# Kernel optimization log

Measured on AMD Instinct MI355X. Metric: run time of the kernel, lower is better.

Reference implementation:

```python
import jax, jax.numpy as jnp
import numpy as np

B, S, D, H = 2, 2048, 1024, 16
HD = D // H

def setup_inputs() -> dict:
    key = jax.random.key(0)
    ks = jax.random.split(key, 6)
    X = jax.random.normal(ks[0], (B, S, D), dtype=jnp.float32)
    mask = jax.random.randint(ks[1], (B, 1, S, S), 0, 2, dtype=jnp.int32)
    scale = 1.0 / np.sqrt(D)
    Wq = jax.random.normal(ks[2], (D, D), dtype=jnp.float32) * scale
    Wk = jax.random.normal(ks[3], (D, D), dtype=jnp.float32) * scale
    Wv = jax.random.normal(ks[4], (D, D), dtype=jnp.float32) * scale
    Wo = jax.random.normal(ks[5], (D, D), dtype=jnp.float32) * scale
    return {"X": X, "mask": mask, "Wq": Wq, "Wk": Wk, "Wv": Wv, "Wo": Wo}

def reference(X, mask, Wq, Wk, Wv, Wo):
    b, s, d = X.shape
    # torch nn.Linear(bias=False): y = x @ W.T, W is [out, in]
    def split_heads(Y):
        return Y.reshape(b, s, H, HD).transpose(0, 2, 1, 3)  # [b,h,s,hd]
    Q = split_heads(X @ Wq.T)
    K = split_heads(X @ Wk.T)
    V = split_heads(X @ Wv.T)
    scores = jnp.einsum('bhqd,bhkd->bhqk', Q, K) / jnp.sqrt(jnp.float32(HD))
    # Faithful to original: masked positions filled with -1e-09 (sic)
    scores = jnp.where(mask == 0, jnp.float32(-1e-09), scores)
    # dropout p=0.0 -> identity (applied to scores pre-softmax in original)
    weights = jax.nn.softmax(scores, axis=-1)
    out = jnp.einsum('bhqk,bhkd->bhqd', weights, V)  # [b,h,s,hd]
    out = out.transpose(0, 2, 1, 3).reshape(b, s, d)
    return out @ Wo.T
```

## Files before the change

### kernel.cpp

```cpp
#include <hip/hip_runtime.h>
#include <hip/hip_bf16.h>

using short8  = __attribute__((ext_vector_type(8))) short;
using f32x4   = __attribute__((ext_vector_type(4))) float;

#if __has_builtin(__builtin_amdgcn_exp2f)
#define EXP2(x) __builtin_amdgcn_exp2f(x)
#else
#define EXP2(x) __expf(0.6931471805599453f*(x))
#endif

__device__ __forceinline__ unsigned short f2bf(float x){
  union { float f; unsigned u; } c; c.f = x;
  unsigned u = c.u + 0x7FFFu + ((c.u >> 16) & 1u);
  return (unsigned short)(u >> 16);
}

__device__ __forceinline__ unsigned pack_bf16_rn(float a, float b){
  __hip_bfloat162 t = __float22bfloat162_rn(make_float2(a, b));
  unsigned u; __builtin_memcpy(&u, &t, 4);
  return u;
}

__global__ __launch_bounds__(256) void prep(const float* __restrict__ X, const int* __restrict__ Mk,
                                            const float* __restrict__ Wq, const float* __restrict__ Wk,
                                            const float* __restrict__ Wv, const float* __restrict__ Wo,
                                            unsigned short* __restrict__ Xb, unsigned short* __restrict__ Wqkv,
                                            unsigned short* __restrict__ Wob, unsigned long long* __restrict__ Mbits)
{
  const int bid = blockIdx.x, tid = threadIdx.x;
  if (bid < 8192){
    const float* src; unsigned short* dst; float scale; int i;
    if (bid < 4096)      { src = X;  dst = Xb;             scale = 1.0f;          i = bid*1024 + tid*4; }
    else if (bid < 5120) { src = Wq; dst = Wqkv;           scale = 0.18033688f;   i = (bid-4096)*1024 + tid*4; }
    else if (bid < 6144) { src = Wk; dst = Wqkv + 1048576; scale = 1.0f;          i = (bid-5120)*1024 + tid*4; }
    else if (bid < 7168) { src = Wv; dst = Wqkv + 2097152; scale = 1.0f;          i = (bid-6144)*1024 + tid*4; }
    else                 { src = Wo; dst = Wob;            scale = 1.0f;          i = (bid-7168)*1024 + tid*4; }
    float4 v = *(const float4*)(src + i);
    ushort4 o;
    o.x = f2bf(v.x * scale); o.y = f2bf(v.y * scale);
    o.z = f2bf(v.z * scale); o.w = f2bf(v.w * scale);
    *(ushort4*)(dst + i) = o;
  } else {
    int row = bid - 8192;
    const int* src = Mk + (size_t)row * 2048;
    unsigned long long* dst = Mbits + (size_t)row * 32;
    int w = tid >> 6, l = tid & 63;
    #pragma unroll
    for (int p = 0; p < 8; p++){
      int v = src[w*512 + p*64 + l];
      unsigned long long bm = __ballot(v != 0);
      if (l == 0) dst[w*8 + p] = bm;
    }
  }
}

__device__ __forceinline__ void stage16(const unsigned short* g, unsigned short* l){
  __builtin_amdgcn_global_load_lds(
      (const __attribute__((address_space(1))) void*)g,
      (__attribute__((address_space(3))) void*)l, 16, 0, 0);
}

__global__ __launch_bounds__(256) void gemm_qkv(const unsigned short* __restrict__ A,
                                                const unsigned short* __restrict__ B,
                                                unsigned short* __restrict__ C,
                                                unsigned short* __restrict__ Vg)
{
  __shared__ unsigned short As[128*32];
  __shared__ unsigned short Bs[128*32];
  const int tid = threadIdx.x;
  const int wave = tid >> 6, lane = tid & 63, l16 = lane & 15, quad = lane >> 4;
  const int id = blockIdx.x, xcd = id & 7, m = id >> 3;
  const int bm = (m / 3) * 128, bn = (xcd * 3 + (m % 3)) * 128;
  const int wm = (wave >> 1) * 64, wn = (wave & 1) * 64;
  const int K = 1024;

  f32x4 acc[4][4] = {};
  for (int k0 = 0; k0 < K; k0 += 32){
    #pragma unroll
    for (int c = 0; c < 2; c++){
      int idx = c * 256 + tid;
      int row = idx >> 2, g = (idx & 3) * 8;
      stage16(A + (size_t)(bm + row) * K + k0 + g, &As[idx * 8]);
      stage16(B + (size_t)(bn + row) * K + k0 + g, &Bs[idx * 8]);
    }
    __syncthreads();
    short8 af[4], bf[4];
    #pragma unroll
    for (int i = 0; i < 4; i++) af[i] = *(const short8*)&As[(wm + i*16 + l16)*32 + quad*8];
    #pragma unroll
    for (int j = 0; j < 4; j++) bf[j] = *(const short8*)&Bs[(wn + j*16 + l16)*32 + quad*8];
    #pragma unroll
    for (int i = 0; i < 4; i++)
      #pragma unroll
      for (int j = 0; j < 4; j++)
        acc[i][j] = __builtin_amdgcn_mfma_f32_16x16x32_bf16(af[i], bf[j], acc[i][j], 0, 0, 0);
    __syncthreads();
  }

  if (bn < 2048){
    #pragma unroll
    for (int i = 0; i < 4; i++){
      int mrow = bm + wm + i*16 + quad*4;
      #pragma unroll
      for (int j = 0; j < 4; j++){
        int ncol = bn + wn + j*16 + l16;
        #pragma unroll
        for (int r = 0; r < 4; r++)
          C[(size_t)(mrow + r) * 3072 + ncol] = f2bf(acc[i][j][r]);
      }
    }
  } else {
    #pragma unroll
    for (int i = 0; i < 4; i++){
      int srow = bm + wm + i*16 + quad*4;
      int b = srow >> 11, s = srow & 2047;
      #pragma unroll
      for (int j = 0; j < 4; j++){
        int c = bn - 2048 + wn + j*16 + l16;
        int h = c >> 6, d = c & 63;
        ushort4 o;
        o.x = f2bf(acc[i][j][0]); o.y = f2bf(acc[i][j][1]);
        o.z = f2bf(acc[i][j][2]); o.w = f2bf(acc[i][j][3]);
        *(ushort4*)&Vg[((size_t)(b*16 + h)*64 + d) * 2048 + s] = o;
      }
    }
  }
}

__global__ __launch_bounds__(256) void gemm_out(const unsigned short* __restrict__ A,
                                                const unsigned short* __restrict__ B,
                                                float* __restrict__ Cf)
{
  __shared__ unsigned short As[128*32];
  __shared__ unsigned short Bs[64*32];
  const int tid = threadIdx.x;
  const int wave = tid >> 6, lane = tid & 63, l16 = lane & 15, quad = lane >> 4;
  const int id = blockIdx.x, xcd = id & 7, m = id >> 3;
  const int bm = (m >> 1) * 128, bn = (xcd * 2 + (m & 1)) * 64;
  const int wm = (wave >> 1) * 64, wn = (wave & 1) * 32;
  const int K = 1024, N = 1024;

  f32x4 acc[4][2] = {};
  for (int k0 = 0; k0 < K; k0 += 32){
    #pragma unroll
    for (int c = 0; c < 2; c++){
      int idx = c * 256 + tid;
      int row = idx >> 2, g = (idx & 3) * 8;
      stage16(A + (size_t)(bm + row) * K + k0 + g, &As[idx * 8]);
    }
    stage16(B + (size_t)(bn + (tid >> 2)) * K + k0 + (tid & 3) * 8, &Bs[tid * 8]);
    __syncthreads();
    short8 af[4], bf[2];
    #pragma unroll
    for (int i = 0; i < 4; i++) af[i] = *(const short8*)&As[(wm + i*16 + l16)*32 + quad*8];
    #pragma unroll
    for (int j = 0; j < 2; j++) bf[j] = *(const short8*)&Bs[(wn + j*16 + l16)*32 + quad*8];
    #pragma unroll
    for (int i = 0; i < 4; i++)
      #pragma unroll
      for (int j = 0; j < 2; j++)
        acc[i][j] = __builtin_amdgcn_mfma_f32_16x16x32_bf16(af[i], bf[j], acc[i][j], 0, 0, 0);
    __syncthreads();
  }
  #pragma unroll
  for (int i = 0; i < 4; i++){
    int mrow = bm + wm + i*16 + quad*4;
    #pragma unroll
    for (int j = 0; j < 2; j++){
      int ncol = bn + wn + j*16 + l16;
      #pragma unroll
      for (int r = 0; r < 4; r++)
        Cf[(size_t)(mrow + r) * N + ncol] = acc[i][j][r];
    }
  }
}

__global__ __launch_bounds__(256, 4) void attn(const unsigned short* __restrict__ QKV,
                                               const unsigned short* __restrict__ Vg,
                                               const unsigned short* __restrict__ mask16,
                                               unsigned short* __restrict__ O)
{
  __shared__ char smem[40960];
  unsigned short* Ks = (unsigned short*)smem;
  unsigned short* Vt = (unsigned short*)(smem + 16384);
  unsigned short* Ps = (unsigned short*)(smem + 32768);
  float* lsums = (float*)smem;

  const int tid = threadIdx.x, wave = tid >> 6, lane = tid & 63;
  const int l16 = lane & 15, quad = lane >> 4;
  const int id = blockIdx.x;
  const int xcd = id & 7, m = id >> 3;
  const int bh = xcd * 4 + (m >> 5);
  const int qblk = (m & 31) * 64;
  const int b = bh >> 4, h = bh & 15;
  const unsigned short* Qg  = QKV + (size_t)b * 2048 * 3072 + h * 64;
  const unsigned short* Kg  = Qg + 1024;
  const unsigned short* Vgb = Vg + (size_t)bh * 64 * 2048;

  const unsigned short* mp[4];
  #pragma unroll
  for (int nt = 0; nt < 4; nt++)
    mp[nt] = mask16 + (size_t)(b*2048 + qblk + nt*16 + l16) * 128 + wave;

  short8 qf[4][2];
  #pragma unroll
  for (int nt = 0; nt < 4; nt++)
    #pragma unroll
    for (int ks = 0; ks < 2; ks++)
      qf[nt][ks] = *(const short8*)(Qg + (size_t)(qblk + nt*16 + l16) * 3072 + ks*32 + quad*8);

  f32x4 oacc[4] = {};
  float plsum[4] = {0.f, 0.f, 0.f, 0.f};
  const int sw = l16 & 7;

  #pragma unroll
  for (int it = 0; it < 2; it++){
    int s = it * 256 + tid;
    int row = s >> 3, bg = (s & 7) ^ (row & 7);
    stage16(Kg + (size_t)row * 3072 + bg * 8, Ks + s * 8);
    stage16(Vgb + (size_t)row * 2048 + bg * 8, Vt + s * 8);
  }
  unsigned mcur[4], mnxt[4] = {0u, 0u, 0u, 0u};
  #pragma unroll
  for (int nt = 0; nt < 4; nt++) mcur[nt] = mp[nt][0];

  for (int c = 0; c < 32; c++){
    const int j0 = c * 64;
    const int buf = (c & 1) * 4096;
    __syncthreads();

    if (c < 31){
      const int nj = j0 + 64, nbuf = ((c + 1) & 1) * 4096;
      #pragma unroll
      for (int it = 0; it < 2; it++){
        int s = it * 256 + tid;
        int row = s >> 3, bg = (s & 7) ^ (row & 7);
        stage16(Kg + (size_t)(nj + row) * 3072 + bg * 8, Ks + nbuf + s * 8);
        stage16(Vgb + (size_t)row * 2048 + nj + bg * 8, Vt + nbuf + s * 8);
      }
      #pragma unroll
      for (int nt = 0; nt < 4; nt++) mnxt[nt] = mp[nt][(c + 1) * 4];
    }

    short8 kf0 = *(const short8*)&Ks[buf + (wave*16 + l16) * 64 + ((0 + quad) ^ sw) * 8];
    short8 kf1 = *(const short8*)&Ks[buf + (wave*16 + l16) * 64 + ((4 + quad) ^ sw) * 8];
    #pragma unroll
    for (int nt = 0; nt < 4; nt++){
      f32x4 a = {0.f, 0.f, 0.f, 0.f};
      __builtin_amdgcn_s_setprio(1);
      a = __builtin_amdgcn_mfma_f32_16x16x32_bf16(kf0, qf[nt][0], a, 0, 0, 0);
      a = __builtin_amdgcn_mfma_f32_16x16x32_bf16(kf1, qf[nt][1], a, 0, 0, 0);
      __builtin_amdgcn_s_setprio(0);
      float p0 = EXP2(a[0]);
      float p1 = EXP2(a[1]);
      float p2 = EXP2(a[2]);
      float p3 = EXP2(a[3]);
      unsigned mq = mcur[nt] >> (quad << 2);
      p0 = (mq & 1u) ? p0 : 1.0f;
      p1 = (mq & 2u) ? p1 : 1.0f;
      p2 = (mq & 4u) ? p2 : 1.0f;
      p3 = (mq & 8u) ? p3 : 1.0f;
      plsum[nt] += (p0 + p1) + (p2 + p3);
      uint2 st; st.x = pack_bf16_rn(p0, p1); st.y = pack_bf16_rn(p2, p3);
      *(uint2*)&Ps[(nt*16 + l16) * 64 + ((wave*2 + (quad >> 1)) ^ sw) * 8 + (quad & 1) * 4] = st;
    }

    __asm__ volatile("s_waitcnt lgkmcnt(0)" ::: "memory");
    __builtin_amdgcn_s_barrier();
    __builtin_amdgcn_sched_barrier(0);

    #pragma unroll
    for (int kk = 0; kk < 2; kk++){
      short8 vfrag = *(const short8*)&Vt[buf + (wave*16 + l16) * 64 + ((kk*4 + quad) ^ sw) * 8];
      short8 pf[4];
      #pragma unroll
      for (int nt = 0; nt < 4; nt++)
        pf[nt] = *(const short8*)&Ps[(nt*16 + l16) * 64 + ((kk*4 + quad) ^ sw) * 8];
      __builtin_amdgcn_s_setprio(1);
      #pragma unroll
      for (int nt = 0; nt < 4; nt++)
        oacc[nt] = __builtin_amdgcn_mfma_f32_16x16x32_bf16(vfrag, pf[nt], oacc[nt], 0, 0, 0);
      __builtin_amdgcn_s_setprio(0);
    }

    #pragma unroll
    for (int nt = 0; nt < 4; nt++) mcur[nt] = mnxt[nt];
  }

  float lw[4];
  #pragma unroll
  for (int nt = 0; nt < 4; nt++){
    float v = plsum[nt];
    v += __shfl_xor(v, 16);
    v += __shfl_xor(v, 32);
    lw[nt] = v;
  }
  __syncthreads();
  if (quad == 0){
    #pragma unroll
    for (int nt = 0; nt < 4; nt++) lsums[(nt*16 + l16) * 4 + wave] = lw[nt];
  }
  __syncthreads();
  float linv[4];
  #pragma unroll
  for (int nt = 0; nt < 4; nt++){
    f32x4 ls = *(const f32x4*)&lsums[(nt*16 + l16) * 4];
    linv[nt] = 1.0f / (ls[0] + ls[1] + ls[2] + ls[3]);
  }
  #pragma unroll
  for (int nt = 0; nt < 4; nt++){
    f32x4 t = oacc[nt];
    unsigned u0 = pack_bf16_rn(t[0] * linv[nt], t[1] * linv[nt]);
    unsigned u1 = pack_bf16_rn(t[2] * linv[nt], t[3] * linv[nt]);
    uint2 st; st.x = u0; st.y = u1;
    *(uint2*)&O[(size_t)(b*2048 + qblk + nt*16 + l16) * 1024 + h*64 + wave*16 + quad*4] = st;
  }
}

extern "C" void kernel_launch(void* const* d_in, const int* in_sizes, int n_in,
                              void* d_out, int out_size, void* d_ws, size_t ws_size,
                              hipStream_t stream)
{
  const float* X  = (const float*)d_in[0];
  const int*   Mk = (const int*)d_in[1];
  const float* Wq = (const float*)d_in[2];
  const float* Wk = (const float*)d_in[3];
  const float* Wv = (const float*)d_in[4];
  const float* Wo = (const float*)d_in[5];
  float* out = (float*)d_out;

  char* ws = (char*)d_ws;
  unsigned short* Xb   = (unsigned short*)(ws + 0);
  unsigned short* Wqkv = (unsigned short*)(ws + 8388608);
  unsigned short* Wob  = (unsigned short*)(ws + 14680064);
  unsigned short* QKV  = (unsigned short*)(ws + 16777216);
  unsigned short* Ob   = (unsigned short*)(ws + 41943040);
  unsigned long long* Mb = (unsigned long long*)(ws + 50331648);
  unsigned short* Vg   = (unsigned short*)(ws + 58720256);

  prep<<<12288, 256, 0, stream>>>(X, Mk, Wq, Wk, Wv, Wo, Xb, Wqkv, Wob, Mb);
  gemm_qkv<<<768, 256, 0, stream>>>(Xb, Wqkv, QKV, Vg);
  attn<<<1024, 256, 0, stream>>>(QKV, Vg, (const unsigned short*)Mb, Ob);
  gemm_out<<<512, 256, 0, stream>>>(Ob, Wob, out);
}
```

Measured before the change: 267.1 us.

## Software-pipeline PV matmul one tile behind and single-buffer K/V in LDS

After: 267.5 us. Within noise of the previous version (+0.2%).

```diff
diff --git a/kernel.cpp b/kernel.cpp
--- a/kernel.cpp
+++ b/kernel.cpp
@@ -181,10 +181,10 @@
                                                const unsigned short* __restrict__ mask16,
                                                unsigned short* __restrict__ O)
 {
-  __shared__ char smem[40960];
+  __shared__ char smem[32768];
   unsigned short* Ks = (unsigned short*)smem;
-  unsigned short* Vt = (unsigned short*)(smem + 16384);
-  unsigned short* Ps = (unsigned short*)(smem + 32768);
+  unsigned short* Vt = (unsigned short*)(smem + 8192);
+  unsigned short* Pb = (unsigned short*)(smem + 16384);
   float* lsums = (float*)smem;
 
   const int tid = threadIdx.x, wave = tid >> 6, lane = tid & 63;
@@ -225,26 +225,34 @@
   #pragma unroll
   for (int nt = 0; nt < 4; nt++) mcur[nt] = mp[nt][0];
 
+  short8 vfp0 = {}, vfp1 = {};
+
   for (int c = 0; c < 32; c++){
-    const int j0 = c * 64;
-    const int buf = (c & 1) * 4096;
-    __syncthreads();
+    __syncthreads();
+
+    const int rbase = (wave*16 + l16) * 64;
+    short8 kf0 = *(const short8*)&Ks[rbase + ((0 + quad) ^ sw) * 8];
+    short8 kf1 = *(const short8*)&Ks[rbase + ((4 + quad) ^ sw) * 8];
+    short8 vf0 = *(const short8*)&Vt[rbase + ((0 + quad) ^ sw) * 8];
+    short8 vf1 = *(const short8*)&Vt[rbase + ((4 + quad) ^ sw) * 8];
+    __asm__ volatile("s_waitcnt lgkmcnt(0)" ::: "memory");
+    __builtin_amdgcn_s_barrier();
+    __builtin_amdgcn_sched_barrier(0);
 
     if (c < 31){
-      const int nj = j0 + 64, nbuf = ((c + 1) & 1) * 4096;
+      const int nj = (c + 1) * 64;
       #pragma unroll
       for (int it = 0; it < 2; it++){
         int s = it * 256 + tid;
         int row = s >> 3, bg = (s & 7) ^ (row & 7);
-        stage16(Kg + (size_t)(nj + row) * 3072 + bg * 8, Ks + nbuf + s * 8);
-        stage16(Vgb + (size_t)row * 2048 + nj + bg * 8, Vt + nbuf + s * 8);
+        stage16(Kg + (size_t)(nj + row) * 3072 + bg * 8, Ks + s * 8);
+        stage16(Vgb + (size_t)row * 2048 + nj + bg * 8, Vt + s * 8);
       }
       #pragma unroll
       for (int nt = 0; nt < 4; nt++) mnxt[nt] = mp[nt][(c + 1) * 4];
     }
 
-    short8 kf0 = *(const short8*)&Ks[buf + (wave*16 + l16) * 64 + ((0 + quad) ^ sw) * 8];
-    short8 kf1 = *(const short8*)&Ks[buf + (wave*16 + l16) * 64 + ((4 + quad) ^ sw) * 8];
+    unsigned short* Pw = Pb + (c & 1) * 4096;
     #pragma unroll
     for (int nt = 0; nt < 4; nt++){
       f32x4 a = {0.f, 0.f, 0.f, 0.f};
@@ -263,29 +271,45 @@
       p3 = (mq & 8u) ? p3 : 1.0f;
       plsum[nt] += (p0 + p1) + (p2 + p3);
       uint2 st; st.x = pack_bf16_rn(p0, p1); st.y = pack_bf16_rn(p2, p3);
-      *(uint2*)&Ps[(nt*16 + l16) * 64 + ((wave*2 + (quad >> 1)) ^ sw) * 8 + (quad & 1) * 4] = st;
-    }
-
-    __asm__ volatile("s_waitcnt lgkmcnt(0)" ::: "memory");
-    __builtin_amdgcn_s_barrier();
-    __builtin_amdgcn_sched_barrier(0);
-
+      *(uint2*)&Pw[(nt*16 + l16) * 64 + ((wave*2 + (quad >> 1)) ^ sw) * 8 + (quad & 1) * 4] = st;
+    }
+
+    if (c){
+      const unsigned short* Pr = Pb + ((c & 1) ^ 1) * 4096;
+      #pragma unroll
+      for (int kk = 0; kk < 2; kk++){
+        short8 vv = kk ? vfp1 : vfp0;
+        short8 pf[4];
+        #pragma unroll
+        for (int nt = 0; nt < 4; nt++)
+          pf[nt] = *(const short8*)&Pr[(nt*16 + l16) * 64 + ((kk*4 + quad) ^ sw) * 8];
+        __builtin_amdgcn_s_setprio(1);
+        #pragma unroll
+        for (int nt = 0; nt < 4; nt++)
+          oacc[nt] = __builtin_amdgcn_mfma_f32_16x16x32_bf16(vv, pf[nt], oacc[nt], 0, 0, 0);
+        __builtin_amdgcn_s_setprio(0);
+      }
+    }
+
+    vfp0 = vf0; vfp1 = vf1;
+    #pragma unroll
+    for (int nt = 0; nt < 4; nt++) mcur[nt] = mnxt[nt];
+  }
+
+  __syncthreads();
+  {
+    const unsigned short* Pr = Pb + 4096;
     #pragma unroll
     for (int kk = 0; kk < 2; kk++){
-      short8 vfrag = *(const short8*)&Vt[buf + (wave*16 + l16) * 64 + ((kk*4 + quad) ^ sw) * 8];
+      short8 vv = kk ? vfp1 : vfp0;
       short8 pf[4];
       #pragma unroll
       for (int nt = 0; nt < 4; nt++)
-        pf[nt] = *(const short8*)&Ps[(nt*16 + l16) * 64 + ((kk*4 + quad) ^ sw) * 8];
-      __builtin_amdgcn_s_setprio(1);
+        pf[nt] = *(const short8*)&Pr[(nt*16 + l16) * 64 + ((kk*4 + quad) ^ sw) * 8];
       #pragma unroll
       for (int nt = 0; nt < 4; nt++)
-        oacc[nt] = __builtin_amdgcn_mfma_f32_16x16x32_bf16(vfrag, pf[nt], oacc[nt], 0, 0, 0);
-      __builtin_amdgcn_s_setprio(0);
-    }
-
-    #pragma unroll
-    for (int nt = 0; nt < 4; nt++) mcur[nt] = mnxt[nt];
+        oacc[nt] = __builtin_amdgcn_mfma_f32_16x16x32_bf16(vv, pf[nt], oacc[nt], 0, 0, 0);
+    }
   }
 
   float lw[4];
```

## Give each wave its own query rows and keep P in registers

Applied to the files above, without the earlier changes.

Result: faster. 241.0 us (-9.8%).

```diff
diff --git a/kernel.cpp b/kernel.cpp
--- a/kernel.cpp
+++ b/kernel.cpp
@@ -2,6 +2,7 @@
 #include <hip/hip_bf16.h>
 
 using short8  = __attribute__((ext_vector_type(8))) short;
+using short4v = __attribute__((ext_vector_type(4))) short;
 using f32x4   = __attribute__((ext_vector_type(4))) float;
 
 #if __has_builtin(__builtin_amdgcn_exp2f)
@@ -44,13 +45,12 @@
   } else {
     int row = bid - 8192;
     const int* src = Mk + (size_t)row * 2048;
-    unsigned long long* dst = Mbits + (size_t)row * 32;
     int w = tid >> 6, l = tid & 63;
     #pragma unroll
     for (int p = 0; p < 8; p++){
       int v = src[w*512 + p*64 + l];
       unsigned long long bm = __ballot(v != 0);
-      if (l == 0) dst[w*8 + p] = bm;
+      if (l == 0) Mbits[(size_t)(w*8 + p) * 4096 + row] = bm;
     }
   }
 }
@@ -178,14 +178,12 @@
 
 __global__ __launch_bounds__(256, 4) void attn(const unsigned short* __restrict__ QKV,
                                                const unsigned short* __restrict__ Vg,
-                                               const unsigned short* __restrict__ mask16,
+                                               const unsigned long long* __restrict__ Mb,
                                                unsigned short* __restrict__ O)
 {
-  __shared__ char smem[40960];
+  __shared__ char smem[32768];
   unsigned short* Ks = (unsigned short*)smem;
   unsigned short* Vt = (unsigned short*)(smem + 16384);
-  unsigned short* Ps = (unsigned short*)(smem + 32768);
-  float* lsums = (float*)smem;
 
   const int tid = threadIdx.x, wave = tid >> 6, lane = tid & 63;
   const int l16 = lane & 15, quad = lane >> 4;
@@ -198,20 +196,14 @@
   const unsigned short* Kg  = Qg + 1024;
   const unsigned short* Vgb = Vg + (size_t)bh * 64 * 2048;
 
-  const unsigned short* mp[4];
-  #pragma unroll
-  for (int nt = 0; nt < 4; nt++)
-    mp[nt] = mask16 + (size_t)(b*2048 + qblk + nt*16 + l16) * 128 + wave;
-
-  short8 qf[4][2];
-  #pragma unroll
-  for (int nt = 0; nt < 4; nt++)
-    #pragma unroll
-    for (int ks = 0; ks < 2; ks++)
-      qf[nt][ks] = *(const short8*)(Qg + (size_t)(qblk + nt*16 + l16) * 3072 + ks*32 + quad*8);
+  const int qrow = qblk + wave*16 + l16;
+  const unsigned long long* mrow = Mb + (size_t)b*2048 + qrow;
+
+  short8 qf0 = *(const short8*)(Qg + (size_t)qrow * 3072 + quad*8);
+  short8 qf1 = *(const short8*)(Qg + (size_t)qrow * 3072 + 32 + quad*8);
 
   f32x4 oacc[4] = {};
-  float plsum[4] = {0.f, 0.f, 0.f, 0.f};
+  float plsum = 0.f;
   const int sw = l16 & 7;
 
   #pragma unroll
@@ -221,17 +213,14 @@
     stage16(Kg + (size_t)row * 3072 + bg * 8, Ks + s * 8);
     stage16(Vgb + (size_t)row * 2048 + bg * 8, Vt + s * 8);
   }
-  unsigned mcur[4], mnxt[4] = {0u, 0u, 0u, 0u};
-  #pragma unroll
-  for (int nt = 0; nt < 4; nt++) mcur[nt] = mp[nt][0];
+  unsigned long long mcur = mrow[0], mnxt = 0ull;
 
   for (int c = 0; c < 32; c++){
-    const int j0 = c * 64;
     const int buf = (c & 1) * 4096;
     __syncthreads();
 
     if (c < 31){
-      const int nj = j0 + 64, nbuf = ((c + 1) & 1) * 4096;
+      const int nj = (c + 1) * 64, nbuf = ((c + 1) & 1) * 4096;
       #pragma unroll
       for (int it = 0; it < 2; it++){
         int s = it * 256 + tid;
@@ -239,83 +228,54 @@
         stage16(Kg + (size_t)(nj + row) * 3072 + bg * 8, Ks + nbuf + s * 8);
         stage16(Vgb + (size_t)row * 2048 + nj + bg * 8, Vt + nbuf + s * 8);
       }
-      #pragma unroll
-      for (int nt = 0; nt < 4; nt++) mnxt[nt] = mp[nt][(c + 1) * 4];
-    }
-
-    short8 kf0 = *(const short8*)&Ks[buf + (wave*16 + l16) * 64 + ((0 + quad) ^ sw) * 8];
-    short8 kf1 = *(const short8*)&Ks[buf + (wave*16 + l16) * 64 + ((4 + quad) ^ sw) * 8];
-    #pragma unroll
-    for (int nt = 0; nt < 4; nt++){
+      mnxt = mrow[(size_t)(c + 1) * 4096];
+    }
+
+    #pragma unroll
+    for (int kb = 0; kb < 4; kb++){
+      const int krow = kb*16 + l16;
+      short8 kf0 = *(const short8*)&Ks[buf + krow*64 + ((0 + quad) ^ sw) * 8];
+      short8 kf1 = *(const short8*)&Ks[buf + krow*64 + ((4 + quad) ^ sw) * 8];
       f32x4 a = {0.f, 0.f, 0.f, 0.f};
       __builtin_amdgcn_s_setprio(1);
-      a = __builtin_amdgcn_mfma_f32_16x16x32_bf16(kf0, qf[nt][0], a, 0, 0, 0);
-      a = __builtin_amdgcn_mfma_f32_16x16x32_bf16(kf1, qf[nt][1], a, 0, 0, 0);
+      a = __builtin_amdgcn_mfma_f32_16x16x32_bf16(kf0, qf0, a, 0, 0, 0);
+      a = __builtin_amdgcn_mfma_f32_16x16x32_bf16(kf1, qf1, a, 0, 0, 0);
       __builtin_amdgcn_s_setprio(0);
-      float p0 = EXP2(a[0]);
-      float p1 = EXP2(a[1]);
-      float p2 = EXP2(a[2]);
-      float p3 = EXP2(a[3]);
-      unsigned mq = mcur[nt] >> (quad << 2);
-      p0 = (mq & 1u) ? p0 : 1.0f;
-      p1 = (mq & 2u) ? p1 : 1.0f;
-      p2 = (mq & 4u) ? p2 : 1.0f;
-      p3 = (mq & 8u) ? p3 : 1.0f;
-      plsum[nt] += (p0 + p1) + (p2 + p3);
-      uint2 st; st.x = pack_bf16_rn(p0, p1); st.y = pack_bf16_rn(p2, p3);
-      *(uint2*)&Ps[(nt*16 + l16) * 64 + ((wave*2 + (quad >> 1)) ^ sw) * 8 + (quad & 1) * 4] = st;
-    }
-
-    __asm__ volatile("s_waitcnt lgkmcnt(0)" ::: "memory");
-    __builtin_amdgcn_s_barrier();
-    __builtin_amdgcn_sched_barrier(0);
-
-    #pragma unroll
-    for (int kk = 0; kk < 2; kk++){
-      short8 vfrag = *(const short8*)&Vt[buf + (wave*16 + l16) * 64 + ((kk*4 + quad) ^ sw) * 8];
-      short8 pf[4];
-      #pragma unroll
-      for (int nt = 0; nt < 4; nt++)
-        pf[nt] = *(const short8*)&Ps[(nt*16 + l16) * 64 + ((kk*4 + quad) ^ sw) * 8];
+      unsigned mm = (unsigned)(mcur >> (kb*16 + quad*4)) & 15u;
+      float p0 = EXP2(a[0]); p0 = (mm & 1u) ? p0 : 1.0f;
+      float p1 = EXP2(a[1]); p1 = (mm & 2u) ? p1 : 1.0f;
+      float p2 = EXP2(a[2]); p2 = (mm & 4u) ? p2 : 1.0f;
+      float p3 = EXP2(a[3]); p3 = (mm & 8u) ? p3 : 1.0f;
+      plsum += (p0 + p1) + (p2 + p3);
+      uint2 pu; pu.x = pack_bf16_rn(p0, p1); pu.y = pack_bf16_rn(p2, p3);
+      short4v pa = *(short4v*)&pu;
       __builtin_amdgcn_s_setprio(1);
       #pragma unroll
-      for (int nt = 0; nt < 4; nt++)
-        oacc[nt] = __builtin_amdgcn_mfma_f32_16x16x32_bf16(vfrag, pf[nt], oacc[nt], 0, 0, 0);
+      for (int ng = 0; ng < 4; ng++){
+        const int vrow = ng*16 + l16;
+        short4v vf = *(const short4v*)&Vt[buf + vrow*64 +
+                       ((kb*2 + (quad >> 1)) ^ sw) * 8 + (quad & 1) * 4];
+        oacc[ng] = __builtin_amdgcn_mfma_f32_16x16x16bf16_1k(pa, vf, oacc[ng], 0, 0, 0);
+      }
       __builtin_amdgcn_s_setprio(0);
     }
-
-    #pragma unroll
-    for (int nt = 0; nt < 4; nt++) mcur[nt] = mnxt[nt];
-  }
-
-  float lw[4];
+    mcur = mnxt;
+  }
+
+  float v = plsum;
+  v += __shfl_xor(v, 16);
+  v += __shfl_xor(v, 32);
+  float linv = 1.0f / v;
+  float lr[4];
   #pragma unroll
-  for (int nt = 0; nt < 4; nt++){
-    float v = plsum[nt];
-    v += __shfl_xor(v, 16);
-    v += __shfl_xor(v, 32);
-    lw[nt] = v;
-  }
-  __syncthreads();
-  if (quad == 0){
-    #pragma unroll
-    for (int nt = 0; nt < 4; nt++) lsums[(nt*16 + l16) * 4 + wave] = lw[nt];
-  }
-  __syncthreads();
-  float linv[4];
+  for (int r = 0; r < 4; r++) lr[r] = __shfl(linv, quad*4 + r);
+
+  unsigned short* Ob = O + (size_t)(b*2048 + qblk + wave*16) * 1024 + h*64;
   #pragma unroll
-  for (int nt = 0; nt < 4; nt++){
-    f32x4 ls = *(const f32x4*)&lsums[(nt*16 + l16) * 4];
-    linv[nt] = 1.0f / (ls[0] + ls[1] + ls[2] + ls[3]);
-  }
-  #pragma unroll
-  for (int nt = 0; nt < 4; nt++){
-    f32x4 t = oacc[nt];
-    unsigned u0 = pack_bf16_rn(t[0] * linv[nt], t[1] * linv[nt]);
-    unsigned u1 = pack_bf16_rn(t[2] * linv[nt], t[3] * linv[nt]);
-    uint2 st; st.x = u0; st.y = u1;
-    *(uint2*)&O[(size_t)(b*2048 + qblk + nt*16 + l16) * 1024 + h*64 + wave*16 + quad*4] = st;
-  }
+  for (int ng = 0; ng < 4; ng++)
+    #pragma unroll
+    for (int r = 0; r < 4; r++)
+      Ob[(size_t)(quad*4 + r) * 1024 + ng*16 + l16] = f2bf(oacc[ng][r] * lr[r]);
 }
 
 extern "C" void kernel_launch(void* const* d_in, const int* in_sizes, int n_in,
@@ -341,6 +301,6 @@
 
   prep<<<12288, 256, 0, stream>>>(X, Mk, Wq, Wk, Wv, Wo, Xb, Wqkv, Wob, Mb);
   gemm_qkv<<<768, 256, 0, stream>>>(Xb, Wqkv, QKV, Vg);
-  attn<<<1024, 256, 0, stream>>>(QKV, Vg, (const unsigned short*)Mb, Ob);
+  attn<<<1024, 256, 0, stream>>>(QKV, Vg, Mb, Ob);
   gemm_out<<<512, 256, 0, stream>>>(Ob, Wob, out);
 }
```
